# Kernel tuning notes

Measured on AMD Instinct MI355X. Metric: run time of the kernel, lower is better.

Reference implementation:

```python
import jax, jax.numpy as jnp
import numpy as np

N_NODES = 100000
N_EDGES = 300000
D_IN = 256
HID = 1024
N_CLASSES = 64


def _linear_params(key, d_in, d_out):
    k1, k2 = jax.random.split(key)
    bound = 1.0 / np.sqrt(d_in)
    W = jax.random.uniform(k1, (d_in, d_out), jnp.float32, -bound, bound)
    b = jax.random.uniform(k2, (d_out,), jnp.float32, -bound, bound)
    return W, b


def setup_inputs() -> dict:
    key = jax.random.key(0)
    ks = jax.random.split(key, 8)
    x = jax.random.normal(ks[0], (N_NODES, D_IN), jnp.float32)
    edge_index = jax.random.randint(ks[1], (2, N_EDGES), 0, N_NODES, jnp.int64)
    W1a, b1a = _linear_params(ks[2], D_IN, HID)
    W1b, b1b = _linear_params(ks[3], HID, HID)
    W2a, b2a = _linear_params(ks[4], HID, HID)
    W2b, b2b = _linear_params(ks[5], HID, HID)
    Wfc, bfc = _linear_params(ks[6], HID, N_CLASSES)
    return {"x": x, "edge_index": edge_index,
            "W1a": W1a, "b1a": b1a, "W1b": W1b, "b1b": b1b,
            "W2a": W2a, "b2a": b2a, "W2b": W2b, "b2b": b2b,
            "Wfc": Wfc, "bfc": bfc}


def _gin_conv(x, src, dst, Wa, ba, Wb, bb):
    # GINConv, eps=0: nn(x + sum_{j in N(i)} x_j); messages flow src -> dst.
    agg = jax.ops.segment_sum(x[src], dst, num_segments=N_NODES)
    h = x + agg
    h = jax.nn.relu(h @ Wa + ba)
    return h @ Wb + bb


def reference(x, edge_index, W1a, b1a, W1b, b1b, W2a, b2a, W2b, b2b, Wfc, bfc):
    src, dst = edge_index[0], edge_index[1]
    h = _gin_conv(x, src, dst, W1a, b1a, W1b, b1b)
    h = jax.nn.relu(h)
    h = _gin_conv(h, src, dst, W2a, b2a, W2b, b2b)
    logits = h @ Wfc + bfc
    return jax.nn.log_softmax(logits, axis=1)
```

## Files before the change

### kernel.cpp

```cpp
#include <hip/hip_runtime.h>
#include <stdint.h>

#define N_NODES 100000
#define N_EDGES 300000
#define D_IN 256
#define HID 1024
#define N_CLASSES 64
#define NSCAN ((N_NODES + 1023) / 1024)

typedef __bf16 bf16x8 __attribute__((ext_vector_type(8)));
typedef float f32x4 __attribute__((ext_vector_type(4)));

__device__ __forceinline__ float bf2f(unsigned short u) {
  union { unsigned int i; float f; } v; v.i = ((unsigned int)u) << 16; return v.f;
}
__device__ __forceinline__ unsigned short f2bf(float f) {
  union { float f; unsigned int i; } v; v.f = f;
  unsigned int u = v.i;
  unsigned int r = (u + 0x7FFFu + ((u >> 16) & 1u)) >> 16;
  return (unsigned short)r;
}

__device__ __forceinline__ void async16(const void* g, void* l) {
  __builtin_amdgcn_global_load_lds(
      (const __attribute__((address_space(1))) void*)g,
      (__attribute__((address_space(3))) void*)l, 16, 0, 0);
}

__global__ void probe_flags(const unsigned short* __restrict__ w,
                            const unsigned int* __restrict__ e,
                            int* __restrict__ flags) {
  __shared__ int cnt;
  __shared__ unsigned int orv;
  if (threadIdx.x == 0) { cnt = 0; orv = 0u; }
  __syncthreads();
  int c = 0;
  for (int i = threadIdx.x; i < 4096; i += 256) {
    unsigned int ex = (w[i] >> 7) & 0xFFu;
    if (ex > 123u) ++c;
  }
  atomicAdd(&cnt, c);
  unsigned int o = 0;
  for (int j = threadIdx.x; j < 1000; j += 256) o |= e[2 * j + 1];
  atomicOr(&orv, o);
  __syncthreads();
  if (threadIdx.x == 0) {
    flags[0] = (cnt > 64) ? 1 : 0;
    flags[1] = (orv == 0u) ? 1 : 0;
  }
}

__global__ void cvt_edges(const unsigned int* __restrict__ ei,
                          int* __restrict__ src32, int* __restrict__ dst32,
                          const int* __restrict__ flags) {
  int i = blockIdx.x * 256 + threadIdx.x;
  if (i >= N_EDGES) return;
  if (flags[1]) {
    src32[i] = (int)ei[2 * i];
    dst32[i] = (int)ei[2 * (size_t)N_EDGES + 2 * i];
  } else {
    src32[i] = (int)ei[i];
    dst32[i] = (int)ei[N_EDGES + i];
  }
}

__global__ void transpose_tile(const void* __restrict__ W,
                               unsigned short* __restrict__ Wt, int K, int N,
                               const int* __restrict__ flags) {
  __shared__ float t[64][65];
  const int n0 = blockIdx.x * 64, k0 = blockIdx.y * 64;
  const int lane = threadIdx.x & 63, rg = threadIdx.x >> 6;
  const bool isf32 = flags[0] != 0;
#pragma unroll
  for (int i = 0; i < 16; ++i) {
    int r = rg * 16 + i;
    long idx = (long)(k0 + r) * N + n0 + lane;
    t[r][lane] = isf32 ? ((const float*)W)[idx]
                       : bf2f(((const unsigned short*)W)[idx]);
  }
  __syncthreads();
#pragma unroll
  for (int i = 0; i < 16; ++i) {
    int r = rg * 16 + i;
    Wt[(long)(n0 + r) * K + k0 + lane] = f2bf(t[lane][r]);
  }
}

__global__ void cvt_bias_all(const void* __restrict__ b1a, const void* __restrict__ b1b,
                             const void* __restrict__ b2a, const void* __restrict__ b2b,
                             const void* __restrict__ bfc,
                             unsigned short* __restrict__ bb,
                             const int* __restrict__ flags) {
  int i = blockIdx.x * 256 + threadIdx.x;
  if (i >= 4 * HID + N_CLASSES) return;
  const void* src; int off;
  if (i < HID)          { src = b1a; off = i; }
  else if (i < 2 * HID) { src = b1b; off = i - HID; }
  else if (i < 3 * HID) { src = b2a; off = i - 2 * HID; }
  else if (i < 4 * HID) { src = b2b; off = i - 3 * HID; }
  else                  { src = bfc; off = i - 4 * HID; }
  bb[i] = flags[0] ? f2bf(((const float*)src)[off])
                   : ((const unsigned short*)src)[off];
}

__global__ void hist_deg(const int* __restrict__ dst, int* __restrict__ deg) {
  int e = blockIdx.x * 256 + threadIdx.x;
  if (e < N_EDGES) atomicAdd(&deg[dst[e]], 1);
}

__global__ void scan_part(const int* __restrict__ deg, int* __restrict__ rowptr,
                          int* __restrict__ bsum) {
  __shared__ int lds[1024];
  int i = blockIdx.x * 1024 + threadIdx.x;
  int v = (i < N_NODES) ? deg[i] : 0;
  lds[threadIdx.x] = v;
  __syncthreads();
  for (int off = 1; off < 1024; off <<= 1) {
    int t = (threadIdx.x >= off) ? lds[threadIdx.x - off] : 0;
    __syncthreads();
    lds[threadIdx.x] += t;
    __syncthreads();
  }
  if (i < N_NODES) rowptr[i + 1] = lds[threadIdx.x];
  if (threadIdx.x == 1023) bsum[blockIdx.x] = lds[1023];
}

__global__ void scan_top(int* __restrict__ bsum) {
  __shared__ int lds[128];
  int v = (threadIdx.x < NSCAN) ? bsum[threadIdx.x] : 0;
  lds[threadIdx.x] = v;
  __syncthreads();
  for (int off = 1; off < 128; off <<= 1) {
    int t = (threadIdx.x >= off) ? lds[threadIdx.x - off] : 0;
    __syncthreads();
    lds[threadIdx.x] += t;
    __syncthreads();
  }
  if (threadIdx.x < NSCAN) bsum[threadIdx.x] = lds[threadIdx.x] - v;
}

__global__ void scan_fix(const int* __restrict__ deg, int* __restrict__ rowptr,
                         int* __restrict__ cursor, const int* __restrict__ bsum) {
  int i = blockIdx.x * 1024 + threadIdx.x;
  if (i < N_NODES) {
    int incl = rowptr[i + 1] + bsum[blockIdx.x];
    rowptr[i + 1] = incl;
    cursor[i] = incl - deg[i];
  }
  if (i == 0) rowptr[0] = 0;
}

__global__ void fill_csr(const int* __restrict__ src, const int* __restrict__ dst,
                         int* __restrict__ cursor, int* __restrict__ csr) {
  int e = blockIdx.x * 256 + threadIdx.x;
  if (e < N_EDGES) {
    int pos = atomicAdd(&cursor[dst[e]], 1);
    csr[pos] = src[e];
  }
}

__global__ void agg1_full(const void* __restrict__ X,
                          const int* __restrict__ rowptr,
                          const int* __restrict__ csr,
                          unsigned short* __restrict__ h,
                          const int* __restrict__ flags) {
  int node = blockIdx.x * 4 + (threadIdx.x >> 6);
  int lane = threadIdx.x & 63;
  if (node >= N_NODES) return;
  bool isf32 = flags[0] != 0;
  float acc[4];
  int e0 = rowptr[node], e1 = rowptr[node + 1];
  if (isf32) {
    const float* Xf = (const float*)X;
    float4 v = ((const float4*)(Xf + (long)node * D_IN))[lane];
    acc[0] = v.x; acc[1] = v.y; acc[2] = v.z; acc[3] = v.w;
    int j = e0;
    for (; j + 3 < e1; j += 4) {
      int s0 = csr[j], s1 = csr[j + 1], s2 = csr[j + 2], s3 = csr[j + 3];
      float4 v0 = ((const float4*)(Xf + (long)s0 * D_IN))[lane];
      float4 v1 = ((const float4*)(Xf + (long)s1 * D_IN))[lane];
      float4 v2 = ((const float4*)(Xf + (long)s2 * D_IN))[lane];
      float4 v3 = ((const float4*)(Xf + (long)s3 * D_IN))[lane];
      acc[0] += v0.x; acc[1] += v0.y; acc[2] += v0.z; acc[3] += v0.w;
      acc[0] += v1.x; acc[1] += v1.y; acc[2] += v1.z; acc[3] += v1.w;
      acc[0] += v2.x; acc[1] += v2.y; acc[2] += v2.z; acc[3] += v2.w;
      acc[0] += v3.x; acc[1] += v3.y; acc[2] += v3.z; acc[3] += v3.w;
    }
    for (; j < e1; ++j) {
      int s = csr[j];
      float4 v0 = ((const float4*)(Xf + (long)s * D_IN))[lane];
      acc[0] += v0.x; acc[1] += v0.y; acc[2] += v0.z; acc[3] += v0.w;
    }
  } else {
    const unsigned short* Xb = (const unsigned short*)X;
    ushort4 v = ((const ushort4*)(Xb + (long)node * D_IN))[lane];
    acc[0] = bf2f(v.x); acc[1] = bf2f(v.y); acc[2] = bf2f(v.z); acc[3] = bf2f(v.w);
    int j = e0;
    for (; j + 3 < e1; j += 4) {
      int s0 = csr[j], s1 = csr[j + 1], s2 = csr[j + 2], s3 = csr[j + 3];
      ushort4 v0 = ((const ushort4*)(Xb + (long)s0 * D_IN))[lane];
      ushort4 v1 = ((const ushort4*)(Xb + (long)s1 * D_IN))[lane];
      ushort4 v2 = ((const ushort4*)(Xb + (long)s2 * D_IN))[lane];
      ushort4 v3 = ((const ushort4*)(Xb + (long)s3 * D_IN))[lane];
      acc[0] += bf2f(v0.x); acc[1] += bf2f(v0.y); acc[2] += bf2f(v0.z); acc[3] += bf2f(v0.w);
      acc[0] += bf2f(v1.x); acc[1] += bf2f(v1.y); acc[2] += bf2f(v1.z); acc[3] += bf2f(v1.w);
      acc[0] += bf2f(v2.x); acc[1] += bf2f(v2.y); acc[2] += bf2f(v2.z); acc[3] += bf2f(v2.w);
      acc[0] += bf2f(v3.x); acc[1] += bf2f(v3.y); acc[2] += bf2f(v3.z); acc[3] += bf2f(v3.w);
    }
    for (; j < e1; ++j) {
      int s = csr[j];
      ushort4 v0 = ((const ushort4*)(Xb + (long)s * D_IN))[lane];
      acc[0] += bf2f(v0.x); acc[1] += bf2f(v0.y); acc[2] += bf2f(v0.z); acc[3] += bf2f(v0.w);
    }
  }
  ushort4 o;
  o.x = f2bf(acc[0]); o.y = f2bf(acc[1]); o.z = f2bf(acc[2]); o.w = f2bf(acc[3]);
  ((ushort4*)(h + (long)node * D_IN))[lane] = o;
}

__global__ void agg2_rot(const unsigned short* __restrict__ Q,
                         const int* __restrict__ rowptr,
                         const int* __restrict__ csr,
                         unsigned short* __restrict__ out, long ostride, int cb) {
  int node = blockIdx.x * 4 + (threadIdx.x >> 6);
  int lane = threadIdx.x & 63;
  if (node >= N_NODES) return;
  unsigned int p = ((const unsigned int*)(Q + (long)node * HID + cb * 128))[lane];
  float a0 = bf2f((unsigned short)(p & 0xFFFFu));
  float a1 = bf2f((unsigned short)(p >> 16));
  int e0 = rowptr[node], e1 = rowptr[node + 1];
  int j = e0;
  for (; j + 1 < e1; j += 2) {
    int s0 = csr[j], s1 = csr[j + 1];
    unsigned int q0 = ((const unsigned int*)(Q + (long)s0 * HID + cb * 128))[lane];
    unsigned int q1 = ((const unsigned int*)(Q + (long)s1 * HID + cb * 128))[lane];
    a0 += bf2f((unsigned short)(q0 & 0xFFFFu));
    a1 += bf2f((unsigned short)(q0 >> 16));
    a0 += bf2f((unsigned short)(q1 & 0xFFFFu));
    a1 += bf2f((unsigned short)(q1 >> 16));
  }
  if (j < e1) {
    int s = csr[j];
    unsigned int q = ((const unsigned int*)(Q + (long)s * HID + cb * 128))[lane];
    a0 += bf2f((unsigned short)(q & 0xFFFFu));
    a1 += bf2f((unsigned short)(q >> 16));
  }
  unsigned int o = (unsigned int)f2bf(a0) | ((unsigned int)f2bf(a1) << 16);
  ((unsigned int*)(out + (long)node * ostride))[lane] = o;
}

__global__ void copyback_cols(unsigned short* __restrict__ Q,
                              const unsigned short* __restrict__ T, int cb) {
  long i = (long)blockIdx.x * 256 + threadIdx.x;
  if (i < (long)N_NODES * 16) {
    long node = i >> 4;
    int c = (int)(i & 15);
    ((uint4*)(Q + node * HID + cb * 128))[c] = ((const uint4*)T)[i];
  }
}

template <int WGM, int WGN, int EPI>
__global__ __launch_bounds__(256, 2) void gemm_bt(
    const unsigned short* __restrict__ A, const unsigned short* __restrict__ Bt,
    const unsigned short* __restrict__ bias, void* __restrict__ Cout,
    int M, int N, int K, int akoff) {
  constexpr int BM = WGM * 64;
  constexpr int BN = WGN * 64;
  __shared__ alignas(16) unsigned short ldsA[BM * 64];
  __shared__ alignas(16) unsigned short ldsB[BN * 64];
  const int tid = threadIdx.x;
  const int lane = tid & 63;
  const int w = tid >> 6;
  const int wm = w % WGM;
  const int wn = w / WGM;
  const long row0 = (long)blockIdx.x * BM;
  const long col0 = (long)blockIdx.y * BN;
  const int l15 = lane & 15, lq = lane >> 4;

  f32x4 acc[4][4];
#pragma unroll
  for (int i = 0; i < 4; ++i)
#pragma unroll
    for (int j = 0; j < 4; ++j) acc[i][j] = f32x4{0.f, 0.f, 0.f, 0.f};

  for (int k0 = 0; k0 < K; k0 += 64) {
    const int ka = (k0 + akoff) & (K - 1);
#pragma unroll
    for (int i = 0; i < BM * 8 / 256; ++i) {
      int t = i * 256 + tid;
      int r = t >> 3, c = t & 7;
      long gr = row0 + r;
      if (gr >= M) gr = M - 1;
      const unsigned short* g = A + gr * (long)K + ka + ((c ^ (r & 7)) << 3);
      void* l = (char*)ldsA + (size_t)(i * 256 + (tid & ~63)) * 16;
      async16(g, l);
    }
#pragma unroll
    for (int i = 0; i < BN * 8 / 256; ++i) {
      int t = i * 256 + tid;
      int r = t >> 3, c = t & 7;
      long gr = col0 + r;
      const unsigned short* g = Bt + gr * (long)K + k0 + ((c ^ (r & 7)) << 3);
      void* l = (char*)ldsB + (size_t)(i * 256 + (tid & ~63)) * 16;
      async16(g, l);
    }
    __syncthreads();
#pragma unroll
    for (int kk = 0; kk < 64; kk += 32) {
      bf16x8 av[4], bv[4];
#pragma unroll
      for (int mt = 0; mt < 4; ++mt) {
        int m = wm * 64 + mt * 16 + l15;
        int jj = ((kk >> 3) + lq) ^ (m & 7);
        av[mt] = *(const bf16x8*)(ldsA + m * 64 + jj * 8);
      }
#pragma unroll
      for (int nt = 0; nt < 4; ++nt) {
        int n = wn * 64 + nt * 16 + l15;
        int jj = ((kk >> 3) + lq) ^ (n & 7);
        bv[nt] = *(const bf16x8*)(ldsB + n * 64 + jj * 8);
      }
#pragma unroll
      for (int mt = 0; mt < 4; ++mt)
#pragma unroll
        for (int nt = 0; nt < 4; ++nt)
          acc[mt][nt] = __builtin_amdgcn_mfma_f32_16x16x32_bf16(
              av[mt], bv[nt], acc[mt][nt], 0, 0, 0);
    }
    __syncthreads();
  }

  if (EPI == 3) {
    float bvx[4];
#pragma unroll
    for (int nt = 0; nt < 4; ++nt) bvx[nt] = bf2f(bias[wn * 64 + nt * 16 + l15]);
#pragma unroll
    for (int mt = 0; mt < 4; ++mt) {
#pragma unroll
      for (int r = 0; r < 4; ++r) {
        long gm = row0 + wm * 64 + mt * 16 + lq * 4 + r;
        float v[4];
#pragma unroll
        for (int nt = 0; nt < 4; ++nt) v[nt] = acc[mt][nt][r] + bvx[nt];
        float mx = fmaxf(fmaxf(v[0], v[1]), fmaxf(v[2], v[3]));
#pragma unroll
        for (int o = 1; o < 16; o <<= 1) mx = fmaxf(mx, __shfl_xor(mx, o, 16));
        float s = expf(v[0] - mx) + expf(v[1] - mx) + expf(v[2] - mx) + expf(v[3] - mx);
#pragma unroll
        for (int o = 1; o < 16; o <<= 1) s += __shfl_xor(s, o, 16);
        float ls = logf(s);
        if (gm < M) {
#pragma unroll
          for (int nt = 0; nt < 4; ++nt)
            ((float*)Cout)[gm * N + nt * 16 + l15] = v[nt] - mx - ls;
        }
      }
    }
    return;
  }

#pragma unroll
  for (int nt = 0; nt < 4; ++nt) {
    long gn = col0 + wn * 64 + nt * 16 + l15;
    float bvl = bf2f(bias[gn]);
#pragma unroll
    for (int mt = 0; mt < 4; ++mt) {
      long gm0 = row0 + wm * 64 + mt * 16 + lq * 4;
#pragma unroll
      for (int r = 0; r < 4; ++r) {
        long gm = gm0 + r;
        if (gm < M) {
          float v = acc[mt][nt][r] + bvl;
          if (EPI == 1) v = v > 0.f ? v : 0.f;
          if (EPI == 2)
            ((float*)Cout)[gm * N + gn] = v;
          else
            ((unsigned short*)Cout)[gm * N + gn] = f2bf(v);
        }
      }
    }
  }
}

extern "C" void kernel_launch(void* const* d_in, const int* in_sizes, int n_in,
                              void* d_out, int out_size, void* d_ws,
                              size_t ws_size, hipStream_t stream) {
  const void* x = d_in[0];
  const unsigned int* ei = (const unsigned int*)d_in[1];
  const void* W1a = d_in[2];
  const void* b1a = d_in[3];
  const void* W1b = d_in[4];
  const void* b1b = d_in[5];
  const void* W2a = d_in[6];
  const void* b2a = d_in[7];
  const void* W2b = d_in[8];
  const void* b2b = d_in[9];
  const void* Wfc = d_in[10];
  const void* bfc = d_in[11];
  (void)n_in; (void)in_sizes; (void)out_size;

  const size_t BIG_NEED = 246909600;
  const bool big = (ws_size >= BIG_NEED);
  const int CMr = big ? 16384 : 8192;
  const int NFULLr = big ? 6 : 12;
  const int TAILR = N_NODES - NFULLr * CMr;

  char* wsb = (char*)d_ws;
  const size_t HOFF = (size_t)N_NODES * (HID - D_IN);
  const size_t AGG_OFF = 204800000;
  const size_t W_OFFv = big ? 238354432 : 233600000;
  const size_t WBYTES = 6946816;
  const size_t B_OFFv = W_OFFv + WBYTES;
  const size_t RP_OFFv = B_OFFv + 8320;
  const size_t CSR_OFFv = RP_OFFv + 400016;
  const size_t F_OFFv = CSR_OFFv + 1200000;
  unsigned short* Q = (unsigned short*)(wsb + 0);
  unsigned short* hQ = Q + HOFF;
  unsigned short* T1 = (unsigned short*)(wsb + AGG_OFF);
  int* src32 = (int*)(wsb + AGG_OFF);
  int* dst32 = src32 + N_EDGES;
  int* deg = dst32 + N_EDGES;
  int* cursor = deg + N_NODES;
  int* bsum = (int*)(wsb + AGG_OFF + 4 * 1024 * 1024);
  unsigned short* W1aT = (unsigned short*)(wsb + W_OFFv);
  unsigned short* W1bT = W1aT + (size_t)D_IN * HID;
  unsigned short* W2aT = W1bT + (size_t)HID * HID;
  unsigned short* W2bT = W2aT + (size_t)HID * HID;
  unsigned short* WfcT = W2bT + (size_t)HID * HID;
  unsigned short* bb1a = (unsigned short*)(wsb + B_OFFv);
  unsigned short* bb1b = bb1a + HID;
  unsigned short* bb2a = bb1b + HID;
  unsigned short* bb2b = bb2a + HID;
  unsigned short* bbfc = bb2b + HID;
  int* rowptr = (int*)(wsb + RP_OFFv);
  int* csr = (int*)(wsb + CSR_OFFv);
  int* flags = (int*)(wsb + F_OFFv);

  probe_flags<<<1, 256, 0, stream>>>((const unsigned short*)W1a, ei, flags);
  cvt_edges<<<(N_EDGES + 255) / 256, 256, 0, stream>>>(ei, src32, dst32, flags);
  hipMemsetAsync(deg, 0, (size_t)N_NODES * 4, stream);
  hist_deg<<<(N_EDGES + 255) / 256, 256, 0, stream>>>(dst32, deg);
  scan_part<<<NSCAN, 1024, 0, stream>>>(deg, rowptr, bsum);
  scan_top<<<1, 128, 0, stream>>>(bsum);
  scan_fix<<<NSCAN, 1024, 0, stream>>>(deg, rowptr, cursor, bsum);
  fill_csr<<<(N_EDGES + 255) / 256, 256, 0, stream>>>(src32, dst32, cursor, csr);
  cvt_bias_all<<<(4 * HID + N_CLASSES + 255) / 256, 256, 0, stream>>>(
      b1a, b1b, b2a, b2b, bfc, bb1a, flags);
  transpose_tile<<<dim3(HID / 64, D_IN / 64), 256, 0, stream>>>(W1a, W1aT, D_IN, HID, flags);
  transpose_tile<<<dim3(HID / 64, HID / 64), 256, 0, stream>>>(W1b, W1bT, HID, HID, flags);
  transpose_tile<<<dim3(HID / 64, HID / 64), 256, 0, stream>>>(W2a, W2aT, HID, HID, flags);
  transpose_tile<<<dim3(HID / 64, HID / 64), 256, 0, stream>>>(W2b, W2bT, HID, HID, flags);
  transpose_tile<<<dim3(N_CLASSES / 64, HID / 64), 256, 0, stream>>>(Wfc, WfcT, HID, N_CLASSES, flags);

  const int ngrid = (N_NODES + 3) / 4;

  agg1_full<<<ngrid, 256, 0, stream>>>(x, rowptr, csr, hQ, flags);

  for (int c = 0; c <= NFULLr; ++c) {
    int rows = (c < NFULLr) ? CMr : TAILR;
    if (rows <= 0) break;
    const unsigned short* Ac = hQ + (size_t)c * CMr * D_IN;
    unsigned short* Qc = Q + (size_t)c * CMr * HID;
    dim3 g((rows + 127) / 128, HID / 128);
    gemm_bt<2, 2, 1><<<g, 256, 0, stream>>>(Ac, W1aT, bb1a, T1, rows, HID, D_IN, 0);
    gemm_bt<2, 2, 1><<<g, 256, 0, stream>>>(T1, W1bT, bb1b, Qc, rows, HID, HID, 0);
  }

  for (int cb = 0; cb < HID / 128; ++cb) {
    if (cb == 0)
      agg2_rot<<<ngrid, 256, 0, stream>>>(Q, rowptr, csr, T1, 128, 0);
    else
      agg2_rot<<<ngrid, 256, 0, stream>>>(Q, rowptr, csr,
                                          Q + (size_t)(cb - 1) * 128, HID, cb);
  }
  const int cgrid = (int)(((long)N_NODES * 16 + 255) / 256);
  copyback_cols<<<cgrid, 256, 0, stream>>>(Q, T1, 7);

  for (int c = 0; c <= NFULLr; ++c) {
    int rows = (c < NFULLr) ? CMr : TAILR;
    if (rows <= 0) break;
    unsigned short* Qc = Q + (size_t)c * CMr * HID;
    dim3 g((rows + 127) / 128, HID / 128);
    gemm_bt<2, 2, 1><<<g, 256, 0, stream>>>(Qc, W2aT, bb2a, T1, rows, HID, HID, 896);
    gemm_bt<2, 2, 0><<<g, 256, 0, stream>>>(T1, W2bT, bb2b, Qc, rows, HID, HID, 0);
  }

  dim3 ghead((N_NODES + 255) / 256, 1);
  gemm_bt<4, 1, 3><<<ghead, 256, 0, stream>>>(
      Q, WfcT, bbfc, (float*)d_out, N_NODES, N_CLASSES, HID, 0);
}
```

Before: 1.573 ms.

## Fold W2b into classifier head weights to skip second-layer output GEMM

Since no nonlinearity sits between the second GIN layer's output linear and the classifier, W2b and Wfc are precomputed into a combined 1024x64 weight (Wcomb = W2b·Wfc) and a combined bias (b2b·Wfc + bfc). The per-chunk N=1024 GEMM for W2b and the separate head pass are replaced by one N=64 head GEMM reading T1 directly. This removes a large 100000x1024x1024 GEMM and the write/read of its output, at the cost of a small precompute and an extra bf16 rounding of the combined weights. Row chunking for layer 2 is changed to 12288-row chunks.

```diff
diff --git a/kernel.cpp b/kernel.cpp
--- a/kernel.cpp
+++ b/kernel.cpp
@@ -64,13 +64,14 @@
   }
 }
 
+template <int FB16>
 __global__ void transpose_tile(const void* __restrict__ W,
                                unsigned short* __restrict__ Wt, int K, int N,
                                const int* __restrict__ flags) {
   __shared__ float t[64][65];
   const int n0 = blockIdx.x * 64, k0 = blockIdx.y * 64;
   const int lane = threadIdx.x & 63, rg = threadIdx.x >> 6;
-  const bool isf32 = flags[0] != 0;
+  const bool isf32 = FB16 ? false : (flags[0] != 0);
 #pragma unroll
   for (int i = 0; i < 16; ++i) {
     int r = rg * 16 + i;
@@ -101,6 +102,18 @@
   else                  { src = bfc; off = i - 4 * HID; }
   bb[i] = flags[0] ? f2bf(((const float*)src)[off])
                    : ((const unsigned short*)src)[off];
+}
+
+__global__ void bcomb_kernel(const unsigned short* __restrict__ bb2b,
+                             const unsigned short* __restrict__ WfcT,
+                             const unsigned short* __restrict__ bbfc,
+                             unsigned short* __restrict__ bcomb) {
+  int c = threadIdx.x;
+  if (c >= N_CLASSES) return;
+  float s = bf2f(bbfc[c]);
+  for (int j = 0; j < HID; ++j)
+    s += bf2f(bb2b[j]) * bf2f(WfcT[(long)c * HID + j]);
+  bcomb[c] = f2bf(s);
 }
 
 __global__ void hist_deg(const int* __restrict__ dst, int* __restrict__ deg) {
@@ -422,6 +435,10 @@
   int* deg = dst32 + N_EDGES;
   int* cursor = deg + N_NODES;
   int* bsum = (int*)(wsb + AGG_OFF + 4 * 1024 * 1024);
+  unsigned short* W2bN = (unsigned short*)(wsb + AGG_OFF + 25600000);
+  unsigned short* WcombT = (unsigned short*)(wsb + AGG_OFF + 25600000 + 2097152);
+  unsigned short* bcomb = WcombT + (size_t)N_CLASSES * HID;
+  unsigned short* zbias = bcomb + 64;
   unsigned short* W1aT = (unsigned short*)(wsb + W_OFFv);
   unsigned short* W1bT = W1aT + (size_t)D_IN * HID;
   unsigned short* W2aT = W1bT + (size_t)HID * HID;
@@ -446,11 +463,11 @@
   fill_csr<<<(N_EDGES + 255) / 256, 256, 0, stream>>>(src32, dst32, cursor, csr);
   cvt_bias_all<<<(4 * HID + N_CLASSES + 255) / 256, 256, 0, stream>>>(
       b1a, b1b, b2a, b2b, bfc, bb1a, flags);
-  transpose_tile<<<dim3(HID / 64, D_IN / 64), 256, 0, stream>>>(W1a, W1aT, D_IN, HID, flags);
-  transpose_tile<<<dim3(HID / 64, HID / 64), 256, 0, stream>>>(W1b, W1bT, HID, HID, flags);
-  transpose_tile<<<dim3(HID / 64, HID / 64), 256, 0, stream>>>(W2a, W2aT, HID, HID, flags);
-  transpose_tile<<<dim3(HID / 64, HID / 64), 256, 0, stream>>>(W2b, W2bT, HID, HID, flags);
-  transpose_tile<<<dim3(N_CLASSES / 64, HID / 64), 256, 0, stream>>>(Wfc, WfcT, HID, N_CLASSES, flags);
+  transpose_tile<0><<<dim3(HID / 64, D_IN / 64), 256, 0, stream>>>(W1a, W1aT, D_IN, HID, flags);
+  transpose_tile<0><<<dim3(HID / 64, HID / 64), 256, 0, stream>>>(W1b, W1bT, HID, HID, flags);
+  transpose_tile<0><<<dim3(HID / 64, HID / 64), 256, 0, stream>>>(W2a, W2aT, HID, HID, flags);
+  transpose_tile<0><<<dim3(HID / 64, HID / 64), 256, 0, stream>>>(W2b, W2bT, HID, HID, flags);
+  transpose_tile<0><<<dim3(N_CLASSES / 64, HID / 64), 256, 0, stream>>>(Wfc, WfcT, HID, N_CLASSES, flags);
 
   const int ngrid = (N_NODES + 3) / 4;
 
@@ -466,6 +483,11 @@
     gemm_bt<2, 2, 1><<<g, 256, 0, stream>>>(T1, W1bT, bb1b, Qc, rows, HID, HID, 0);
   }
 
+  hipMemsetAsync(zbias, 0, 2048, stream);
+  transpose_tile<1><<<dim3(HID / 64, HID / 64), 256, 0, stream>>>(W2bT, W2bN, HID, HID, flags);
+  gemm_bt<1, 4, 0><<<dim3(1, 4), 256, 0, stream>>>(WfcT, W2bN, zbias, WcombT, 64, HID, HID, 0);
+  bcomb_kernel<<<1, 64, 0, stream>>>(bb2b, WfcT, bbfc, bcomb);
+
   for (int cb = 0; cb < HID / 128; ++cb) {
     if (cb == 0)
       agg2_rot<<<ngrid, 256, 0, stream>>>(Q, rowptr, csr, T1, 128, 0);
@@ -476,16 +498,16 @@
   const int cgrid = (int)(((long)N_NODES * 16 + 255) / 256);
   copyback_cols<<<cgrid, 256, 0, stream>>>(Q, T1, 7);
 
-  for (int c = 0; c <= NFULLr; ++c) {
-    int rows = (c < NFULLr) ? CMr : TAILR;
+  const int CH2 = 12288, NF2 = 8;
+  for (int c = 0; c <= NF2; ++c) {
+    int rows = (c < NF2) ? CH2 : (N_NODES - NF2 * CH2);
     if (rows <= 0) break;
-    unsigned short* Qc = Q + (size_t)c * CMr * HID;
+    unsigned short* Qc = Q + (size_t)c * CH2 * HID;
     dim3 g((rows + 127) / 128, HID / 128);
     gemm_bt<2, 2, 1><<<g, 256, 0, stream>>>(Qc, W2aT, bb2a, T1, rows, HID, HID, 896);
-    gemm_bt<2, 2, 0><<<g, 256, 0, stream>>>(T1, W2bT, bb2b, Qc, rows, HID, HID, 0);
-  }
-
-  dim3 ghead((N_NODES + 255) / 256, 1);
-  gemm_bt<4, 1, 3><<<ghead, 256, 0, stream>>>(
-      Q, WfcT, bbfc, (float*)d_out, N_NODES, N_CLASSES, HID, 0);
-}
+    dim3 gh((rows + 255) / 256, 1);
+    gemm_bt<4, 1, 3><<<gh, 256, 0, stream>>>(
+        T1, WcombT, bcomb, (float*)d_out + (size_t)c * CH2 * N_CLASSES,
+        rows, N_CLASSES, HID, 0);
+  }
+}
```

New measurement: 1.574 ms. Within noise of the previous version (+0.1%).
